# Kernel tuning notes

Measured on AMD Instinct MI355X. Metric: run time of the kernel, lower is better.

The kernel has to match this reference:

```python
import jax, jax.numpy as jnp
import numpy as np

N_INPUTS = 4
ACTIVE_IDX = 0
EPS = 1e-6


def _rmsnorm(x, w, eps=EPS):
    v = jnp.mean(x * x, axis=-1, keepdims=True)
    return x * jax.lax.rsqrt(v + eps) * w


def setup_inputs() -> dict:
    key = jax.random.key(0)
    ks = jax.random.split(key, 7)
    N, B, S, H = N_INPUTS, 4, 2048, 2048
    return {
        "hidden_states": jax.random.normal(ks[0], (N, B, S, H), dtype=jnp.float32),
        "activated": jax.random.normal(ks[1], (B, S, H), dtype=jnp.float32),
        "router_norm_weight": 1.0 + 0.02 * jax.random.normal(ks[2], (H,), dtype=jnp.float32),
        "modality_router_w": 0.02 * jax.random.normal(ks[3], (N, H), dtype=jnp.float32),
        "prediction_w": 0.02 * jax.random.normal(ks[4], (N * N, N), dtype=jnp.float32),
        "correction_w": 0.02 * jax.random.normal(ks[5], (N, N), dtype=jnp.float32),
        "correct_output_scale": 0.02 * jax.random.normal(ks[6], (H,), dtype=jnp.float32),
    }


def reference(hidden_states, activated, router_norm_weight, modality_router_w,
              prediction_w, correction_w, correct_output_scale):
    N, B, S, H = hidden_states.shape
    router_input_scale = 1.0 / H

    def modalities(x):  # x: [B,S,H] -> [B,S,N]
        ri = _rmsnorm(x, router_norm_weight) * router_input_scale
        routed = jnp.einsum('bsh,nh->bsn', ri, modality_router_w)
        return jnp.tanh(routed.astype(jnp.float32)).astype(x.dtype)

    # ---- predict ----
    m = modalities(hidden_states[ACTIVE_IDX])                    # [B,S,N]
    coefs = jnp.einsum('bsn,kn->bsk', m, prediction_w)           # [B,S,N*N]
    coefs = coefs.reshape(B, S, N, N)                            # raw[b,s,j,i]
    # torch: permute last two then matmul -> pred[j] = sum_i hs[i]*raw[...,j,i]
    predictions = jnp.einsum('ibsh,bsji->jbsh', hidden_states, coefs) + hidden_states

    # ---- correct ----
    m2 = modalities(activated)                                   # [B,S,N]
    innovation = activated - predictions[ACTIVE_IDX]             # [B,S,H]
    ccoefs = jnp.einsum('bsn,kn->bsk', m2, correction_w) + 1.0   # [B,S,N]
    ccoefs = jnp.transpose(ccoefs, (2, 0, 1))[..., None]         # [N,B,S,1]
    corrected = innovation[None] * ccoefs + predictions          # [N,B,S,H]

    # ---- scale_corrected_output ----
    return corrected * correct_output_scale
```

## Files before the change

### kernel.cpp

```cpp
#include <hip/hip_runtime.h>
#include <math.h>

#define HDIM 2048
#define THREADS 256
#define VEC (HDIM / (THREADS * 4))

typedef float v4f __attribute__((ext_vector_type(4)));

__global__ __launch_bounds__(THREADS, 4)
void altup_kernel(const float* __restrict__ hs,
                  const float* __restrict__ act,
                  const float* __restrict__ rnw,
                  const float* __restrict__ mrw,
                  const float* __restrict__ pw,
                  const float* __restrict__ cw,
                  const float* __restrict__ scale,
                  float* __restrict__ out,
                  int T)
{
    const int t = blockIdx.x;
    const int tid = threadIdx.x;
    const size_t row = (size_t)t * HDIM;
    const size_t plane = (size_t)T * HDIM;

    const v4f* hs0p = (const v4f*)(hs + row);
    const v4f* actp = (const v4f*)(act + row);
    const v4f* wp   = (const v4f*)rnw;
    const v4f* mrp  = (const v4f*)mrw;

    v4f x0v[VEC], av[VEC];
    float acc[10];
    #pragma unroll
    for (int k = 0; k < 10; ++k) acc[k] = 0.f;

    #pragma unroll
    for (int v = 0; v < VEC; ++v) {
        const int idx = tid + v * THREADS;
        const v4f x  = __builtin_nontemporal_load(hs0p + idx);
        const v4f a  = __builtin_nontemporal_load(actp + idx);
        const v4f ww = wp[idx];
        x0v[v] = x; av[v] = a;
        acc[0] += x.x*x.x + x.y*x.y + x.z*x.z + x.w*x.w;
        acc[5] += a.x*a.x + a.y*a.y + a.z*a.z + a.w*a.w;
        const float xwx = x.x*ww.x, xwy = x.y*ww.y, xwz = x.z*ww.z, xww = x.w*ww.w;
        const float awx = a.x*ww.x, awy = a.y*ww.y, awz = a.z*ww.z, aww = a.w*ww.w;
        #pragma unroll
        for (int n = 0; n < 4; ++n) {
            const v4f r = mrp[n * (HDIM/4) + idx];
            acc[1+n] += xwx*r.x + xwy*r.y + xwz*r.z + xww*r.w;
            acc[6+n] += awx*r.x + awy*r.y + awz*r.z + aww*r.w;
        }
    }

    const v4f* h1p = (const v4f*)(hs + plane + row);
    const v4f* h2p = (const v4f*)(hs + 2*plane + row);
    const v4f* h3p = (const v4f*)(hs + 3*plane + row);
    const v4f* scp = (const v4f*)scale;
    v4f x1v[VEC], x2v[VEC], x3v[VEC], scv[VEC];
    #pragma unroll
    for (int v = 0; v < VEC; ++v) {
        const int idx = tid + v * THREADS;
        x1v[v] = __builtin_nontemporal_load(h1p + idx);
        x2v[v] = __builtin_nontemporal_load(h2p + idx);
        x3v[v] = __builtin_nontemporal_load(h3p + idx);
        scv[v] = scp[idx];
    }

    __shared__ float part[THREADS/64][10];
    const int lane = tid & 63, wv = tid >> 6;
    #pragma unroll
    for (int k = 0; k < 10; ++k) {
        float s = acc[k];
        #pragma unroll
        for (int off = 32; off >= 1; off >>= 1) s += __shfl_down(s, off, 64);
        if (lane == 0) part[wv][k] = s;
    }
    __syncthreads();
    float tot[10];
    #pragma unroll
    for (int k = 0; k < 10; ++k)
        tot[k] = part[0][k] + part[1][k] + part[2][k] + part[3][k];

    const float invH = 1.0f / HDIM;
    const float rs0 = rsqrtf(tot[0] * invH + 1e-6f) * invH;
    const float rsA = rsqrtf(tot[5] * invH + 1e-6f) * invH;
    float m0[4], m2[4];
    #pragma unroll
    for (int n = 0; n < 4; ++n) {
        m0[n] = tanhf(tot[1+n] * rs0);
        m2[n] = tanhf(tot[6+n] * rsA);
    }
    float c[4][4], cc[4];
    #pragma unroll
    for (int j = 0; j < 4; ++j) {
        #pragma unroll
        for (int i = 0; i < 4; ++i) {
            const float* p = pw + (j*4 + i) * 4;
            c[j][i] = p[0]*m0[0] + p[1]*m0[1] + p[2]*m0[2] + p[3]*m0[3]
                    + (i == j ? 1.f : 0.f);
        }
        const float* q = cw + j*4;
        cc[j] = 1.f + q[0]*m2[0] + q[1]*m2[1] + q[2]*m2[2] + q[3]*m2[3];
    }

    float* o0 = out + row;
    float* o1 = out + plane + row;
    float* o2 = out + 2*plane + row;
    float* o3 = out + 3*plane + row;

    #pragma unroll
    for (int v = 0; v < VEC; ++v) {
        const int idx = tid + v * THREADS;
        const v4f x0 = x0v[v];
        const v4f a  = av[v];
        const v4f x1 = x1v[v];
        const v4f x2 = x2v[v];
        const v4f x3 = x3v[v];
        const v4f sc = scv[v];
        v4f r0, r1, r2, r3;
        #define COMP(f) { \
            const float p0 = c[0][0]*x0.f + c[0][1]*x1.f + c[0][2]*x2.f + c[0][3]*x3.f; \
            const float p1 = c[1][0]*x0.f + c[1][1]*x1.f + c[1][2]*x2.f + c[1][3]*x3.f; \
            const float p2 = c[2][0]*x0.f + c[2][1]*x1.f + c[2][2]*x2.f + c[2][3]*x3.f; \
            const float p3 = c[3][0]*x0.f + c[3][1]*x1.f + c[3][2]*x2.f + c[3][3]*x3.f; \
            const float inn = a.f - p0; \
            r0.f = (p0 + inn*cc[0]) * sc.f; \
            r1.f = (p1 + inn*cc[1]) * sc.f; \
            r2.f = (p2 + inn*cc[2]) * sc.f; \
            r3.f = (p3 + inn*cc[3]) * sc.f; }
        COMP(x) COMP(y) COMP(z) COMP(w)
        #undef COMP
        __builtin_nontemporal_store(r0, (v4f*)(o0) + idx);
        __builtin_nontemporal_store(r1, (v4f*)(o1) + idx);
        __builtin_nontemporal_store(r2, (v4f*)(o2) + idx);
        __builtin_nontemporal_store(r3, (v4f*)(o3) + idx);
    }
}

extern "C" void kernel_launch(void* const* d_in, const int* in_sizes, int n_in,
                              void* d_out, int out_size, void* d_ws, size_t ws_size,
                              hipStream_t stream) {
    const float* hs  = (const float*)d_in[0];
    const float* act = (const float*)d_in[1];
    const float* rnw = (const float*)d_in[2];
    const float* mrw = (const float*)d_in[3];
    const float* pw  = (const float*)d_in[4];
    const float* cw  = (const float*)d_in[5];
    const float* sc  = (const float*)d_in[6];
    float* out = (float*)d_out;

    const int T = in_sizes[1] / HDIM;
    altup_kernel<<<T, THREADS, 0, stream>>>(hs, act, rnw, mrw, pw, cw, sc, out, T);
}
```

Baseline: 472.3 us.

## Process one token row per wavefront and defer loading of remaining planes

Each 64-lane wavefront now owns a whole token row, so the row reductions use xor shuffles with no shared memory or block barrier. The loads of hidden-state planes 1-3 and the scale vector move from before the reduction into the output loop, which lowers register pressure. Launch bounds drop from 4 to 3 blocks, since each thread now holds 8 vectors per array instead of 2. The cost is less memory parallelism in flight per thread before the reduction, and the later loads are no longer overlapped with the reduction math.

Measured after the change: 499.1 us. +5.7%, slower.

```diff
diff --git a/kernel.cpp b/kernel.cpp
--- a/kernel.cpp
+++ b/kernel.cpp
@@ -3,11 +3,11 @@
 
 #define HDIM 2048
 #define THREADS 256
-#define VEC (HDIM / (THREADS * 4))
+#define WPT (HDIM / (64 * 4))
 
 typedef float v4f __attribute__((ext_vector_type(4)));
 
-__global__ __launch_bounds__(THREADS, 4)
+__global__ __launch_bounds__(THREADS, 3)
 void altup_kernel(const float* __restrict__ hs,
                   const float* __restrict__ act,
                   const float* __restrict__ rnw,
@@ -18,9 +18,12 @@
                   float* __restrict__ out,
                   int T)
 {
-    const int t = blockIdx.x;
-    const int tid = threadIdx.x;
-    const size_t row = (size_t)t * HDIM;
+    const int lane = (int)(threadIdx.x & 63);
+    const int wv   = (int)(threadIdx.x >> 6);
+    const int t    = blockIdx.x * 4 + wv;
+    if (t >= T) return;
+
+    const size_t row   = (size_t)t * HDIM;
     const size_t plane = (size_t)T * HDIM;
 
     const v4f* hs0p = (const v4f*)(hs + row);
@@ -28,14 +31,14 @@
     const v4f* wp   = (const v4f*)rnw;
     const v4f* mrp  = (const v4f*)mrw;
 
-    v4f x0v[VEC], av[VEC];
+    v4f x0v[WPT], av[WPT];
     float acc[10];
     #pragma unroll
     for (int k = 0; k < 10; ++k) acc[k] = 0.f;
 
     #pragma unroll
-    for (int v = 0; v < VEC; ++v) {
-        const int idx = tid + v * THREADS;
+    for (int v = 0; v < WPT; ++v) {
+        const int idx = lane + v * 64;
         const v4f x  = __builtin_nontemporal_load(hs0p + idx);
         const v4f a  = __builtin_nontemporal_load(actp + idx);
         const v4f ww = wp[idx];
@@ -52,34 +55,14 @@
         }
     }
 
-    const v4f* h1p = (const v4f*)(hs + plane + row);
-    const v4f* h2p = (const v4f*)(hs + 2*plane + row);
-    const v4f* h3p = (const v4f*)(hs + 3*plane + row);
-    const v4f* scp = (const v4f*)scale;
-    v4f x1v[VEC], x2v[VEC], x3v[VEC], scv[VEC];
-    #pragma unroll
-    for (int v = 0; v < VEC; ++v) {
-        const int idx = tid + v * THREADS;
-        x1v[v] = __builtin_nontemporal_load(h1p + idx);
-        x2v[v] = __builtin_nontemporal_load(h2p + idx);
-        x3v[v] = __builtin_nontemporal_load(h3p + idx);
-        scv[v] = scp[idx];
-    }
-
-    __shared__ float part[THREADS/64][10];
-    const int lane = tid & 63, wv = tid >> 6;
+    float tot[10];
     #pragma unroll
     for (int k = 0; k < 10; ++k) {
         float s = acc[k];
         #pragma unroll
-        for (int off = 32; off >= 1; off >>= 1) s += __shfl_down(s, off, 64);
-        if (lane == 0) part[wv][k] = s;
+        for (int off = 1; off < 64; off <<= 1) s += __shfl_xor(s, off, 64);
+        tot[k] = s;
     }
-    __syncthreads();
-    float tot[10];
-    #pragma unroll
-    for (int k = 0; k < 10; ++k)
-        tot[k] = part[0][k] + part[1][k] + part[2][k] + part[3][k];
 
     const float invH = 1.0f / HDIM;
     const float rs0 = rsqrtf(tot[0] * invH + 1e-6f) * invH;
@@ -103,20 +86,24 @@
         cc[j] = 1.f + q[0]*m2[0] + q[1]*m2[1] + q[2]*m2[2] + q[3]*m2[3];
     }
 
+    const v4f* h1p = (const v4f*)(hs + plane + row);
+    const v4f* h2p = (const v4f*)(hs + 2*plane + row);
+    const v4f* h3p = (const v4f*)(hs + 3*plane + row);
+    const v4f* scp = (const v4f*)scale;
     float* o0 = out + row;
     float* o1 = out + plane + row;
     float* o2 = out + 2*plane + row;
     float* o3 = out + 3*plane + row;
 
     #pragma unroll
-    for (int v = 0; v < VEC; ++v) {
-        const int idx = tid + v * THREADS;
+    for (int v = 0; v < WPT; ++v) {
+        const int idx = lane + v * 64;
+        const v4f x1 = __builtin_nontemporal_load(h1p + idx);
+        const v4f x2 = __builtin_nontemporal_load(h2p + idx);
+        const v4f x3 = __builtin_nontemporal_load(h3p + idx);
+        const v4f sc = scp[idx];
         const v4f x0 = x0v[v];
         const v4f a  = av[v];
-        const v4f x1 = x1v[v];
-        const v4f x2 = x2v[v];
-        const v4f x3 = x3v[v];
-        const v4f sc = scv[v];
         v4f r0, r1, r2, r3;
         #define COMP(f) { \
             const float p0 = c[0][0]*x0.f + c[0][1]*x1.f + c[0][2]*x2.f + c[0][3]*x3.f; \
@@ -150,5 +137,6 @@
     float* out = (float*)d_out;
 
     const int T = in_sizes[1] / HDIM;
-    altup_kernel<<<T, THREADS, 0, stream>>>(hs, act, rnw, mrw, pw, cw, sc, out, T);
+    const int nb = (T + 3) / 4;
+    altup_kernel<<<nb, THREADS, 0, stream>>>(hs, act, rnw, mrw, pw, cw, sc, out, T);
 }
```

## Split fused kernel into coefficient pass and streaming combine pass

Applied to the files above, without the earlier changes.

Computes the per-token routing coefficients in a separate kernel that writes them to workspace, then runs a lightweight streaming kernel that reads them and combines all planes. This removes the need to hold hidden-state rows in registers across the block reduction, lowering register pressure and allowing more waves in flight. It costs rereading the active hidden-state plane and activated input, plus an extra launch. The original fused kernel remains as a fallback when workspace is insufficient.

After: 517.2 us. +9.5%, slower.

```diff
diff --git a/kernel.cpp b/kernel.cpp
--- a/kernel.cpp
+++ b/kernel.cpp
@@ -4,35 +4,169 @@
 #define HDIM 2048
 #define THREADS 256
 #define VEC (HDIM / (THREADS * 4))
+#define COEF_STRIDE 32
 
 typedef float v4f __attribute__((ext_vector_type(4)));
 
+__global__ __launch_bounds__(THREADS, 8)
+void coef_kernel(const float* __restrict__ hs,
+                 const float* __restrict__ act,
+                 const float* __restrict__ rnw,
+                 const float* __restrict__ mrw,
+                 const float* __restrict__ pw,
+                 const float* __restrict__ cw,
+                 float* __restrict__ coefs,
+                 int T)
+{
+    const int t = blockIdx.x;
+    const int tid = threadIdx.x;
+    const size_t row = (size_t)t * HDIM;
+
+    const v4f* hs0p = (const v4f*)(hs + row);
+    const v4f* actp = (const v4f*)(act + row);
+    const v4f* wp   = (const v4f*)rnw;
+    const v4f* mrp  = (const v4f*)mrw;
+
+    float acc[10];
+    #pragma unroll
+    for (int k = 0; k < 10; ++k) acc[k] = 0.f;
+
+    #pragma unroll
+    for (int v = 0; v < VEC; ++v) {
+        const int idx = tid + v * THREADS;
+        const v4f x  = __builtin_nontemporal_load(hs0p + idx);
+        const v4f a  = __builtin_nontemporal_load(actp + idx);
+        const v4f ww = wp[idx];
+        acc[0] += x.x*x.x + x.y*x.y + x.z*x.z + x.w*x.w;
+        acc[5] += a.x*a.x + a.y*a.y + a.z*a.z + a.w*a.w;
+        const float xwx = x.x*ww.x, xwy = x.y*ww.y, xwz = x.z*ww.z, xww = x.w*ww.w;
+        const float awx = a.x*ww.x, awy = a.y*ww.y, awz = a.z*ww.z, aww = a.w*ww.w;
+        #pragma unroll
+        for (int n = 0; n < 4; ++n) {
+            const v4f r = mrp[n * (HDIM/4) + idx];
+            acc[1+n] += xwx*r.x + xwy*r.y + xwz*r.z + xww*r.w;
+            acc[6+n] += awx*r.x + awy*r.y + awz*r.z + aww*r.w;
+        }
+    }
+
+    __shared__ float part[THREADS/64][10];
+    const int lane = tid & 63, wv = tid >> 6;
+    #pragma unroll
+    for (int k = 0; k < 10; ++k) {
+        float s = acc[k];
+        #pragma unroll
+        for (int off = 32; off >= 1; off >>= 1) s += __shfl_down(s, off, 64);
+        if (lane == 0) part[wv][k] = s;
+    }
+    __syncthreads();
+    if (tid >= 64) return;
+    float tot[10];
+    #pragma unroll
+    for (int k = 0; k < 10; ++k)
+        tot[k] = part[0][k] + part[1][k] + part[2][k] + part[3][k];
+
+    const float invH = 1.0f / HDIM;
+    const float rs0 = rsqrtf(tot[0] * invH + 1e-6f) * invH;
+    const float rsA = rsqrtf(tot[5] * invH + 1e-6f) * invH;
+    float m0[4], m2[4];
+    #pragma unroll
+    for (int n = 0; n < 4; ++n) {
+        m0[n] = tanhf(tot[1+n] * rs0);
+        m2[n] = tanhf(tot[6+n] * rsA);
+    }
+    float* cf = coefs + (size_t)t * COEF_STRIDE;
+    if (tid < 16) {
+        const int j = tid >> 2, i = tid & 3;
+        const float* p = pw + (j*4 + i) * 4;
+        cf[tid] = p[0]*m0[0] + p[1]*m0[1] + p[2]*m0[2] + p[3]*m0[3]
+                + (i == j ? 1.f : 0.f);
+    } else if (tid < 20) {
+        const int j = tid - 16;
+        const float* q = cw + j*4;
+        cf[tid] = 1.f + q[0]*m2[0] + q[1]*m2[1] + q[2]*m2[2] + q[3]*m2[3];
+    }
+}
+
+__global__ __launch_bounds__(THREADS, 6)
+void combine_kernel(const float* __restrict__ hs,
+                    const float* __restrict__ act,
+                    const float* __restrict__ scale,
+                    const float* __restrict__ coefs,
+                    float* __restrict__ out,
+                    int T)
+{
+    const int t = blockIdx.x;
+    const int tid = threadIdx.x;
+    const size_t row   = (size_t)t * HDIM;
+    const size_t plane = (size_t)T * HDIM;
+
+    const float* cf = coefs + (size_t)t * COEF_STRIDE;
+    float c[4][4], cc[4];
+    #pragma unroll
+    for (int j = 0; j < 4; ++j) {
+        #pragma unroll
+        for (int i = 0; i < 4; ++i) c[j][i] = cf[j*4 + i];
+        cc[j] = cf[16 + j];
+    }
+
+    const v4f* h0p = (const v4f*)(hs + row);
+    const v4f* h1p = (const v4f*)(hs + plane + row);
+    const v4f* h2p = (const v4f*)(hs + 2*plane + row);
+    const v4f* h3p = (const v4f*)(hs + 3*plane + row);
+    const v4f* actp = (const v4f*)(act + row);
+    const v4f* scp  = (const v4f*)scale;
+    float* o0 = out + row;
+    float* o1 = out + plane + row;
+    float* o2 = out + 2*plane + row;
+    float* o3 = out + 3*plane + row;
+
+    #pragma unroll
+    for (int v = 0; v < VEC; ++v) {
+        const int idx = tid + v * THREADS;
+        const v4f x0 = __builtin_nontemporal_load(h0p + idx);
+        const v4f x1 = __builtin_nontemporal_load(h1p + idx);
+        const v4f x2 = __builtin_nontemporal_load(h2p + idx);
+        const v4f x3 = __builtin_nontemporal_load(h3p + idx);
+        const v4f a  = __builtin_nontemporal_load(actp + idx);
+        const v4f sc = scp[idx];
+        v4f r0, r1, r2, r3;
+        #define COMP(f) { \
+            const float p0 = c[0][0]*x0.f + c[0][1]*x1.f + c[0][2]*x2.f + c[0][3]*x3.f; \
+            const float p1 = c[1][0]*x0.f + c[1][1]*x1.f + c[1][2]*x2.f + c[1][3]*x3.f; \
+            const float p2 = c[2][0]*x0.f + c[2][1]*x1.f + c[2][2]*x2.f + c[2][3]*x3.f; \
+            const float p3 = c[3][0]*x0.f + c[3][1]*x1.f + c[3][2]*x2.f + c[3][3]*x3.f; \
+            const float inn = a.f - p0; \
+            r0.f = (p0 + inn*cc[0]) * sc.f; \
+            r1.f = (p1 + inn*cc[1]) * sc.f; \
+            r2.f = (p2 + inn*cc[2]) * sc.f; \
+            r3.f = (p3 + inn*cc[3]) * sc.f; }
+        COMP(x) COMP(y) COMP(z) COMP(w)
+        #undef COMP
+        __builtin_nontemporal_store(r0, (v4f*)(o0) + idx);
+        __builtin_nontemporal_store(r1, (v4f*)(o1) + idx);
+        __builtin_nontemporal_store(r2, (v4f*)(o2) + idx);
+        __builtin_nontemporal_store(r3, (v4f*)(o3) + idx);
+    }
+}
+
 __global__ __launch_bounds__(THREADS, 4)
-void altup_kernel(const float* __restrict__ hs,
-                  const float* __restrict__ act,
-                  const float* __restrict__ rnw,
-                  const float* __restrict__ mrw,
-                  const float* __restrict__ pw,
-                  const float* __restrict__ cw,
-                  const float* __restrict__ scale,
-                  float* __restrict__ out,
-                  int T)
+void altup_fused(const float* __restrict__ hs, const float* __restrict__ act,
+                 const float* __restrict__ rnw, const float* __restrict__ mrw,
+                 const float* __restrict__ pw, const float* __restrict__ cw,
+                 const float* __restrict__ scale, float* __restrict__ out, int T)
 {
     const int t = blockIdx.x;
     const int tid = threadIdx.x;
     const size_t row = (size_t)t * HDIM;
     const size_t plane = (size_t)T * HDIM;
-
     const v4f* hs0p = (const v4f*)(hs + row);
     const v4f* actp = (const v4f*)(act + row);
     const v4f* wp   = (const v4f*)rnw;
     const v4f* mrp  = (const v4f*)mrw;
-
     v4f x0v[VEC], av[VEC];
     float acc[10];
     #pragma unroll
     for (int k = 0; k < 10; ++k) acc[k] = 0.f;
-
     #pragma unroll
     for (int v = 0; v < VEC; ++v) {
         const int idx = tid + v * THREADS;
@@ -51,7 +185,6 @@
             acc[6+n] += awx*r.x + awy*r.y + awz*r.z + aww*r.w;
         }
     }
-
     const v4f* h1p = (const v4f*)(hs + plane + row);
     const v4f* h2p = (const v4f*)(hs + 2*plane + row);
     const v4f* h3p = (const v4f*)(hs + 3*plane + row);
@@ -65,7 +198,6 @@
         x3v[v] = __builtin_nontemporal_load(h3p + idx);
         scv[v] = scp[idx];
     }
-
     __shared__ float part[THREADS/64][10];
     const int lane = tid & 63, wv = tid >> 6;
     #pragma unroll
@@ -80,7 +212,6 @@
     #pragma unroll
     for (int k = 0; k < 10; ++k)
         tot[k] = part[0][k] + part[1][k] + part[2][k] + part[3][k];
-
     const float invH = 1.0f / HDIM;
     const float rs0 = rsqrtf(tot[0] * invH + 1e-6f) * invH;
     const float rsA = rsqrtf(tot[5] * invH + 1e-6f) * invH;
@@ -102,12 +233,10 @@
         const float* q = cw + j*4;
         cc[j] = 1.f + q[0]*m2[0] + q[1]*m2[1] + q[2]*m2[2] + q[3]*m2[3];
     }
-
     float* o0 = out + row;
     float* o1 = out + plane + row;
     float* o2 = out + 2*plane + row;
     float* o3 = out + 3*plane + row;
-
     #pragma unroll
     for (int v = 0; v < VEC; ++v) {
         const int idx = tid + v * THREADS;
@@ -150,5 +279,13 @@
     float* out = (float*)d_out;
 
     const int T = in_sizes[1] / HDIM;
-    altup_kernel<<<T, THREADS, 0, stream>>>(hs, act, rnw, mrw, pw, cw, sc, out, T);
-}
+    const size_t need = (size_t)T * COEF_STRIDE * sizeof(float);
+
+    if (d_ws != nullptr && ws_size >= need) {
+        float* coefs = (float*)d_ws;
+        coef_kernel<<<T, THREADS, 0, stream>>>(hs, act, rnw, mrw, pw, cw, coefs, T);
+        combine_kernel<<<T, THREADS, 0, stream>>>(hs, act, sc, coefs, out, T);
+    } else {
+        altup_fused<<<T, THREADS, 0, stream>>>(hs, act, rnw, mrw, pw, cw, sc, out, T);
+    }
+}
```

## Make blocks persistent over row chunks with prefetch of next row

Applied to the files above, without the earlier changes.

Launches at most 1024 blocks, each handling a contiguous chunk of tokens, and prefetches the next row's hidden_states[0] and activated vectors while the current row is reduced and written. The other three hidden-state planes are now loaded inside the output loop instead of being held in registers up front. The aim is to cut block launch overhead and hide load latency behind the reduction. In exchange there are fewer resident waves for latency hiding, an extra barrier per row, and the loads of the other planes become more serialized.

Result: slower. 507.7 us (+7.5%).

```diff
diff --git a/kernel.cpp b/kernel.cpp
--- a/kernel.cpp
+++ b/kernel.cpp
@@ -4,6 +4,7 @@
 #define HDIM 2048
 #define THREADS 256
 #define VEC (HDIM / (THREADS * 4))
+#define MAXB 1024
 
 typedef float v4f __attribute__((ext_vector_type(4)));
 
@@ -16,124 +17,146 @@
                   const float* __restrict__ cw,
                   const float* __restrict__ scale,
                   float* __restrict__ out,
-                  int T)
+                  int T, int chunk)
 {
-    const int t = blockIdx.x;
     const int tid = threadIdx.x;
-    const size_t row = (size_t)t * HDIM;
+    const int t0 = blockIdx.x * chunk;
+    const int t1 = (t0 + chunk < T) ? (t0 + chunk) : T;
+    if (t0 >= t1) return;
+
     const size_t plane = (size_t)T * HDIM;
+    const v4f* wp  = (const v4f*)rnw;
+    const v4f* mrp = (const v4f*)mrw;
+    const v4f* scp = (const v4f*)scale;
 
-    const v4f* hs0p = (const v4f*)(hs + row);
-    const v4f* actp = (const v4f*)(act + row);
-    const v4f* wp   = (const v4f*)rnw;
-    const v4f* mrp  = (const v4f*)mrw;
+    __shared__ float part[THREADS/64][10];
+    const int lane = tid & 63, wv = tid >> 6;
 
     v4f x0v[VEC], av[VEC];
-    float acc[10];
-    #pragma unroll
-    for (int k = 0; k < 10; ++k) acc[k] = 0.f;
-
-    #pragma unroll
-    for (int v = 0; v < VEC; ++v) {
-        const int idx = tid + v * THREADS;
-        const v4f x  = __builtin_nontemporal_load(hs0p + idx);
-        const v4f a  = __builtin_nontemporal_load(actp + idx);
-        const v4f ww = wp[idx];
-        x0v[v] = x; av[v] = a;
-        acc[0] += x.x*x.x + x.y*x.y + x.z*x.z + x.w*x.w;
-        acc[5] += a.x*a.x + a.y*a.y + a.z*a.z + a.w*a.w;
-        const float xwx = x.x*ww.x, xwy = x.y*ww.y, xwz = x.z*ww.z, xww = x.w*ww.w;
-        const float awx = a.x*ww.x, awy = a.y*ww.y, awz = a.z*ww.z, aww = a.w*ww.w;
+    {
+        const size_t row = (size_t)t0 * HDIM;
+        const v4f* hs0p = (const v4f*)(hs + row);
+        const v4f* actp = (const v4f*)(act + row);
         #pragma unroll
-        for (int n = 0; n < 4; ++n) {
-            const v4f r = mrp[n * (HDIM/4) + idx];
-            acc[1+n] += xwx*r.x + xwy*r.y + xwz*r.z + xww*r.w;
-            acc[6+n] += awx*r.x + awy*r.y + awz*r.z + aww*r.w;
+        for (int v = 0; v < VEC; ++v) {
+            const int idx = tid + v * THREADS;
+            x0v[v] = __builtin_nontemporal_load(hs0p + idx);
+            av[v]  = __builtin_nontemporal_load(actp + idx);
         }
     }
 
-    const v4f* h1p = (const v4f*)(hs + plane + row);
-    const v4f* h2p = (const v4f*)(hs + 2*plane + row);
-    const v4f* h3p = (const v4f*)(hs + 3*plane + row);
-    const v4f* scp = (const v4f*)scale;
-    v4f x1v[VEC], x2v[VEC], x3v[VEC], scv[VEC];
-    #pragma unroll
-    for (int v = 0; v < VEC; ++v) {
-        const int idx = tid + v * THREADS;
-        x1v[v] = __builtin_nontemporal_load(h1p + idx);
-        x2v[v] = __builtin_nontemporal_load(h2p + idx);
-        x3v[v] = __builtin_nontemporal_load(h3p + idx);
-        scv[v] = scp[idx];
-    }
+    for (int t = t0; t < t1; ++t) {
+        const size_t row = (size_t)t * HDIM;
 
-    __shared__ float part[THREADS/64][10];
-    const int lane = tid & 63, wv = tid >> 6;
-    #pragma unroll
-    for (int k = 0; k < 10; ++k) {
-        float s = acc[k];
+        float acc[10];
         #pragma unroll
-        for (int off = 32; off >= 1; off >>= 1) s += __shfl_down(s, off, 64);
-        if (lane == 0) part[wv][k] = s;
-    }
-    __syncthreads();
-    float tot[10];
-    #pragma unroll
-    for (int k = 0; k < 10; ++k)
-        tot[k] = part[0][k] + part[1][k] + part[2][k] + part[3][k];
+        for (int k = 0; k < 10; ++k) acc[k] = 0.f;
 
-    const float invH = 1.0f / HDIM;
-    const float rs0 = rsqrtf(tot[0] * invH + 1e-6f) * invH;
-    const float rsA = rsqrtf(tot[5] * invH + 1e-6f) * invH;
-    float m0[4], m2[4];
-    #pragma unroll
-    for (int n = 0; n < 4; ++n) {
-        m0[n] = tanhf(tot[1+n] * rs0);
-        m2[n] = tanhf(tot[6+n] * rsA);
-    }
-    float c[4][4], cc[4];
-    #pragma unroll
-    for (int j = 0; j < 4; ++j) {
         #pragma unroll
-        for (int i = 0; i < 4; ++i) {
-            const float* p = pw + (j*4 + i) * 4;
-            c[j][i] = p[0]*m0[0] + p[1]*m0[1] + p[2]*m0[2] + p[3]*m0[3]
-                    + (i == j ? 1.f : 0.f);
+        for (int v = 0; v < VEC; ++v) {
+            const int idx = tid + v * THREADS;
+            const v4f x  = x0v[v];
+            const v4f a  = av[v];
+            const v4f ww = wp[idx];
+            acc[0] += x.x*x.x + x.y*x.y + x.z*x.z + x.w*x.w;
+            acc[5] += a.x*a.x + a.y*a.y + a.z*a.z + a.w*a.w;
+            const float xwx = x.x*ww.x, xwy = x.y*ww.y, xwz = x.z*ww.z, xww = x.w*ww.w;
+            const float awx = a.x*ww.x, awy = a.y*ww.y, awz = a.z*ww.z, aww = a.w*ww.w;
+            #pragma unroll
+            for (int n = 0; n < 4; ++n) {
+                const v4f r = mrp[n * (HDIM/4) + idx];
+                acc[1+n] += xwx*r.x + xwy*r.y + xwz*r.z + xww*r.w;
+                acc[6+n] += awx*r.x + awy*r.y + awz*r.z + aww*r.w;
+            }
         }
-        const float* q = cw + j*4;
-        cc[j] = 1.f + q[0]*m2[0] + q[1]*m2[1] + q[2]*m2[2] + q[3]*m2[3];
-    }
 
-    float* o0 = out + row;
-    float* o1 = out + plane + row;
-    float* o2 = out + 2*plane + row;
-    float* o3 = out + 3*plane + row;
+        v4f nx0[VEC], na[VEC];
+        if (t + 1 < t1) {
+            const size_t nrow = row + HDIM;
+            const v4f* hs0p = (const v4f*)(hs + nrow);
+            const v4f* actp = (const v4f*)(act + nrow);
+            #pragma unroll
+            for (int v = 0; v < VEC; ++v) {
+                const int idx = tid + v * THREADS;
+                nx0[v] = __builtin_nontemporal_load(hs0p + idx);
+                na[v]  = __builtin_nontemporal_load(actp + idx);
+            }
+        }
 
-    #pragma unroll
-    for (int v = 0; v < VEC; ++v) {
-        const int idx = tid + v * THREADS;
-        const v4f x0 = x0v[v];
-        const v4f a  = av[v];
-        const v4f x1 = x1v[v];
-        const v4f x2 = x2v[v];
-        const v4f x3 = x3v[v];
-        const v4f sc = scv[v];
-        v4f r0, r1, r2, r3;
-        #define COMP(f) { \
-            const float p0 = c[0][0]*x0.f + c[0][1]*x1.f + c[0][2]*x2.f + c[0][3]*x3.f; \
-            const float p1 = c[1][0]*x0.f + c[1][1]*x1.f + c[1][2]*x2.f + c[1][3]*x3.f; \
-            const float p2 = c[2][0]*x0.f + c[2][1]*x1.f + c[2][2]*x2.f + c[2][3]*x3.f; \
-            const float p3 = c[3][0]*x0.f + c[3][1]*x1.f + c[3][2]*x2.f + c[3][3]*x3.f; \
-            const float inn = a.f - p0; \
-            r0.f = (p0 + inn*cc[0]) * sc.f; \
-            r1.f = (p1 + inn*cc[1]) * sc.f; \
-            r2.f = (p2 + inn*cc[2]) * sc.f; \
-            r3.f = (p3 + inn*cc[3]) * sc.f; }
-        COMP(x) COMP(y) COMP(z) COMP(w)
-        #undef COMP
-        __builtin_nontemporal_store(r0, (v4f*)(o0) + idx);
-        __builtin_nontemporal_store(r1, (v4f*)(o1) + idx);
-        __builtin_nontemporal_store(r2, (v4f*)(o2) + idx);
-        __builtin_nontemporal_store(r3, (v4f*)(o3) + idx);
+        #pragma unroll
+        for (int k = 0; k < 10; ++k) {
+            float s = acc[k];
+            #pragma unroll
+            for (int off = 32; off >= 1; off >>= 1) s += __shfl_down(s, off, 64);
+            if (lane == 0) part[wv][k] = s;
+        }
+        __syncthreads();
+        float tot[10];
+        #pragma unroll
+        for (int k = 0; k < 10; ++k)
+            tot[k] = part[0][k] + part[1][k] + part[2][k] + part[3][k];
+        __syncthreads();
+
+        const float invH = 1.0f / HDIM;
+        const float rs0 = rsqrtf(tot[0] * invH + 1e-6f) * invH;
+        const float rsA = rsqrtf(tot[5] * invH + 1e-6f) * invH;
+        float m0[4], m2[4];
+        #pragma unroll
+        for (int n = 0; n < 4; ++n) {
+            m0[n] = tanhf(tot[1+n] * rs0);
+            m2[n] = tanhf(tot[6+n] * rsA);
+        }
+        float c[4][4], cc[4];
+        #pragma unroll
+        for (int j = 0; j < 4; ++j) {
+            #pragma unroll
+            for (int i = 0; i < 4; ++i) {
+                const float* p = pw + (j*4 + i) * 4;
+                c[j][i] = p[0]*m0[0] + p[1]*m0[1] + p[2]*m0[2] + p[3]*m0[3]
+                        + (i == j ? 1.f : 0.f);
+            }
+            const float* q = cw + j*4;
+            cc[j] = 1.f + q[0]*m2[0] + q[1]*m2[1] + q[2]*m2[2] + q[3]*m2[3];
+        }
+
+        const v4f* h1p = (const v4f*)(hs + plane + row);
+        const v4f* h2p = (const v4f*)(hs + 2*plane + row);
+        const v4f* h3p = (const v4f*)(hs + 3*plane + row);
+        float* o0 = out + row;
+        float* o1 = out + plane + row;
+        float* o2 = out + 2*plane + row;
+        float* o3 = out + 3*plane + row;
+
+        #pragma unroll
+        for (int v = 0; v < VEC; ++v) {
+            const int idx = tid + v * THREADS;
+            const v4f x1 = __builtin_nontemporal_load(h1p + idx);
+            const v4f x2 = __builtin_nontemporal_load(h2p + idx);
+            const v4f x3 = __builtin_nontemporal_load(h3p + idx);
+            const v4f sc = scp[idx];
+            const v4f x0 = x0v[v];
+            const v4f a  = av[v];
+            v4f r0, r1, r2, r3;
+            #define COMP(f) { \
+                const float p0 = c[0][0]*x0.f + c[0][1]*x1.f + c[0][2]*x2.f + c[0][3]*x3.f; \
+                const float p1 = c[1][0]*x0.f + c[1][1]*x1.f + c[1][2]*x2.f + c[1][3]*x3.f; \
+                const float p2 = c[2][0]*x0.f + c[2][1]*x1.f + c[2][2]*x2.f + c[2][3]*x3.f; \
+                const float p3 = c[3][0]*x0.f + c[3][1]*x1.f + c[3][2]*x2.f + c[3][3]*x3.f; \
+                const float inn = a.f - p0; \
+                r0.f = (p0 + inn*cc[0]) * sc.f; \
+                r1.f = (p1 + inn*cc[1]) * sc.f; \
+                r2.f = (p2 + inn*cc[2]) * sc.f; \
+                r3.f = (p3 + inn*cc[3]) * sc.f; }
+            COMP(x) COMP(y) COMP(z) COMP(w)
+            #undef COMP
+            __builtin_nontemporal_store(r0, (v4f*)(o0) + idx);
+            __builtin_nontemporal_store(r1, (v4f*)(o1) + idx);
+            __builtin_nontemporal_store(r2, (v4f*)(o2) + idx);
+            __builtin_nontemporal_store(r3, (v4f*)(o3) + idx);
+        }
+
+        #pragma unroll
+        for (int v = 0; v < VEC; ++v) { x0v[v] = nx0[v]; av[v] = na[v]; }
     }
 }
 
@@ -150,5 +173,8 @@
     float* out = (float*)d_out;
 
     const int T = in_sizes[1] / HDIM;
-    altup_kernel<<<T, THREADS, 0, stream>>>(hs, act, rnw, mrw, pw, cw, sc, out, T);
+    int nb = (T < MAXB) ? T : MAXB;
+    const int chunk = (T + nb - 1) / nb;
+    nb = (T + chunk - 1) / chunk;
+    altup_kernel<<<nb, THREADS, 0, stream>>>(hs, act, rnw, mrw, pw, cw, sc, out, T, chunk);
 }
```
